# Performance work log

Hardware: AMD Instinct MI355X
Metric: run time of the kernel (lower is better)

## Reference

```python
import jax, jax.numpy as jnp
import numpy as np

NUM_HEADS = 8
AREA = 4
EPS = 1e-5  # torch BatchNorm2d default


def _conv1x1(x, w):
    # x: [B,C,H,W], w: [O,C] -> [B,O,H,W]
    return jnp.einsum('bchw,oc->bohw', x, w)


def _bn(y, g, b, m, v):
    # inference-mode BatchNorm2d, per-channel affine
    s = g / jnp.sqrt(v + EPS)
    return y * s[None, :, None, None] + (b - m * s)[None, :, None, None]


def setup_inputs() -> dict:
    key = jax.random.key(0)
    ks = jax.random.split(key, 16)
    B, C, H, W = 2, 256, 64, 64
    d = {}
    d['x'] = jax.random.normal(ks[0], (B, C, H, W), jnp.float32)
    # qk conv (dim -> 2*dim) + BN
    d['w_qk'] = jax.random.normal(ks[1], (2 * C, C), jnp.float32) * 0.06
    d['g_qk'] = jax.random.uniform(ks[2], (2 * C,), jnp.float32, 0.5, 1.5)
    d['b_qk'] = jax.random.normal(ks[3], (2 * C,), jnp.float32) * 0.1
    d['m_qk'] = jax.random.normal(ks[4], (2 * C,), jnp.float32) * 0.1
    d['v_qk'] = jax.random.uniform(ks[5], (2 * C,), jnp.float32, 0.5, 1.5)
    # v conv (dim -> dim) + BN
    d['w_v'] = jax.random.normal(ks[6], (C, C), jnp.float32) * 0.06
    d['g_v'] = jax.random.uniform(ks[7], (C,), jnp.float32, 0.5, 1.5)
    d['b_v'] = jax.random.normal(ks[8], (C,), jnp.float32) * 0.1
    d['m_v'] = jax.random.normal(ks[9], (C,), jnp.float32) * 0.1
    d['v_v'] = jax.random.uniform(ks[10], (C,), jnp.float32, 0.5, 1.5)
    # proj conv (dim -> dim) + BN
    d['w_p'] = jax.random.normal(ks[11], (C, C), jnp.float32) * 0.06
    d['g_p'] = jax.random.uniform(ks[12], (C,), jnp.float32, 0.5, 1.5)
    d['b_p'] = jax.random.normal(ks[13], (C,), jnp.float32) * 0.1
    d['m_p'] = jax.random.normal(ks[14], (C,), jnp.float32) * 0.1
    d['v_p'] = jax.random.uniform(ks[15], (C,), jnp.float32, 0.5, 1.5)
    return d


def reference(x, w_qk, g_qk, b_qk, m_qk, v_qk,
              w_v, g_v, b_v, m_v, v_v,
              w_p, g_p, b_p, m_p, v_p):
    B, C, H, W = x.shape
    N = H * W
    hd = C // NUM_HEADS

    qk = _bn(_conv1x1(x, w_qk), g_qk, b_qk, m_qk, v_qk)          # [B,2C,H,W]
    qk = qk.reshape(B, 2 * C, N).transpose(0, 2, 1)               # [B,N,2C]
    vv = _bn(_conv1x1(x, w_v), g_v, b_v, m_v, v_v)                # [B,C,H,W]
    vv = vv.reshape(B, C, N).transpose(0, 2, 1)                   # [B,N,C]

    Ba, Na = B * AREA, N // AREA
    qk = qk.reshape(Ba, Na, 2 * C)
    vv = vv.reshape(Ba, Na, C)
    q, k = qk[..., :C], qk[..., C:]

    # [Ba,Na,C] -> [Ba,heads,hd,Na] (matches torch transpose(1,2).view)
    q = q.reshape(Ba, Na, NUM_HEADS, hd).transpose(0, 2, 3, 1)
    k = k.reshape(Ba, Na, NUM_HEADS, hd).transpose(0, 2, 3, 1)
    v = vv.reshape(Ba, Na, NUM_HEADS, hd).transpose(0, 2, 3, 1)

    scale = hd ** -0.5
    attn = jnp.einsum('bhdi,bhdj->bhij', q, k) * scale            # [Ba,h,Na,Na]
    attn = jax.nn.softmax(attn, axis=-1)                          # max-sub exp/sum
    out = jnp.einsum('bhdj,bhij->bihd', v, attn)                  # [Ba,Na,h,hd]

    out = out.reshape(B, N, C).reshape(B, H, W, C).transpose(0, 3, 1, 2)
    return _bn(_conv1x1(out, w_p), g_p, b_p, m_p, v_p)            # [B,C,H,W]
```

## Files before the change

kernel.cpp:

```cpp
#include <hip/hip_runtime.h>
#include <hip/hip_bf16.h>
#include <math.h>

#define CCH   256
#define NPIX  4096
#define NHD   8
#define HD    32
#define NA    1024
#define BN_EPS 1e-5f
#define ATT_SCALE (0.17677669529663687f * 1.4426950408889634f)

typedef __attribute__((ext_vector_type(8))) short bf16x8;
typedef __attribute__((ext_vector_type(4))) short bf16x4;
typedef __attribute__((ext_vector_type(4))) float f32x4;

static __device__ inline short f2bf(float f) {
    union { float f; unsigned u; } v; v.f = f;
    unsigned r = (v.u + 0x7fff + ((v.u >> 16) & 1)) >> 16;
    return (short)r;
}

static __device__ inline unsigned int pk2bf(float a, float b) {
    __hip_bfloat162 h2 = __float22bfloat162_rn(make_float2(a, b));
    union { __hip_bfloat162 h; unsigned int u; } v; v.h = h2;
    return v.u;
}

__global__ __launch_bounds__(256)
void xt_kernel(const float* __restrict__ x, short* __restrict__ Xt) {
    __shared__ short tile[64][66];
    const int t  = threadIdx.x;
    const int n0 = blockIdx.x << 6;
    const int c0 = blockIdx.y << 6;
    const int b  = blockIdx.z;
    const float* xp = x + (((size_t)(b * CCH + c0)) << 12) + n0;
    #pragma unroll
    for (int j = 0; j < 16; ++j) {
        const int lin = (j << 8) + t;
        const int cl = lin >> 6, nl = lin & 63;
        tile[cl][nl] = f2bf(xp[((size_t)cl << 12) + nl]);
    }
    __syncthreads();
    short* xtp = Xt + ((((size_t)b << 12) + n0) << 8) + c0;
    #pragma unroll
    for (int j = 0; j < 16; ++j) {
        const int lin = (j << 8) + t;
        const int nl = lin >> 6, cl = lin & 63;
        xtp[((size_t)nl << 8) + cl] = tile[cl][nl];
    }
}

__global__ __launch_bounds__(256)
void wcast_kernel(const float* __restrict__ wqk, const float* __restrict__ wv,
                  const float* __restrict__ wp, short* __restrict__ Wb) {
    const int idx = (blockIdx.x * 256 + threadIdx.x) * 4;
    const float* src; int off;
    if (idx < 131072)      { src = wqk; off = idx; }
    else if (idx < 196608) { src = wv;  off = idx - 131072; }
    else                   { src = wp;  off = idx - 196608; }
    const float4 v = *(const float4*)(src + off);
    short4 o;
    o.x = f2bf(v.x); o.y = f2bf(v.y); o.z = f2bf(v.z); o.w = f2bf(v.w);
    *(short4*)(Wb + idx) = o;
}

__global__ __launch_bounds__(256)
void qk_gemm(const short* __restrict__ Xt, const short* __restrict__ Wb,
             const float* __restrict__ g_qk, const float* __restrict__ b_qk,
             const float* __restrict__ m_qk, const float* __restrict__ v_qk,
             short* __restrict__ Qb, short* __restrict__ Kb) {
    const int lane = threadIdx.x & 63;
    const int w    = threadIdx.x >> 6;
    const int c    = lane & 15;
    const int quad = lane >> 4;
    const int m0 = blockIdx.x * 64 + (w >> 1) * 32;
    const int n0 = blockIdx.y * 128 + (w & 1) * 64;

    const short* ap = Xt + ((size_t)(m0 + c) << 8) + (quad << 3);
    const short* bp = Wb + ((size_t)(n0 + c) << 8) + (quad << 3);

    f32x4 acc[2][4];
    #pragma unroll
    for (int f = 0; f < 2; ++f)
        #pragma unroll
        for (int g = 0; g < 4; ++g) acc[f][g] = (f32x4){0.f, 0.f, 0.f, 0.f};

    #pragma unroll
    for (int k = 0; k < 256; k += 32) {
        bf16x8 af[2], bg[4];
        #pragma unroll
        for (int f = 0; f < 2; ++f) af[f] = *(const bf16x8*)(ap + f * 4096 + k);
        #pragma unroll
        for (int g = 0; g < 4; ++g) bg[g] = *(const bf16x8*)(bp + g * 4096 + k);
        #pragma unroll
        for (int f = 0; f < 2; ++f)
            #pragma unroll
            for (int g = 0; g < 4; ++g)
                acc[f][g] = __builtin_amdgcn_mfma_f32_16x16x32_bf16(af[f], bg[g], acc[f][g], 0, 0, 0);
    }

    const bool isQ = (n0 < 256);
    short* dst = isQ ? Qb : Kb;
    const float fold = isQ ? ATT_SCALE : 1.0f;
    #pragma unroll
    for (int g = 0; g < 4; ++g) {
        const int o  = n0 + g * 16 + c;
        const int cd = o & 255;
        const int h  = cd >> 5;
        const int d  = cd & 31;
        float s    = g_qk[o] * rsqrtf(v_qk[o] + BN_EPS);
        float beta = (b_qk[o] - m_qk[o] * s) * fold;
        s *= fold;
        #pragma unroll
        for (int f = 0; f < 2; ++f) {
            #pragma unroll
            for (int r = 0; r < 4; ++r) {
                const int row  = m0 + f * 16 + (quad << 2) + r;
                const int pair = (row >> 10) * NHD + h;
                const int i    = row & 1023;
                dst[(((size_t)pair << 10) + i) * HD + d] = f2bf(acc[f][g][r] * s + beta);
            }
        }
    }
}

__global__ __launch_bounds__(256)
void v_gemm(const short* __restrict__ Wv, const short* __restrict__ Xt,
            const float* __restrict__ g_v, const float* __restrict__ b_v,
            const float* __restrict__ m_v, const float* __restrict__ v_v,
            short* __restrict__ Vb) {
    const int lane = threadIdx.x & 63;
    const int w    = threadIdx.x >> 6;
    const int c    = lane & 15;
    const int quad = lane >> 4;
    const int m0 = blockIdx.x * 64 + (w >> 1) * 32;
    const int n0 = blockIdx.y * 128 + (w & 1) * 64;

    const short* ap = Wv + ((size_t)(m0 + c) << 8) + (quad << 3);
    const short* bp = Xt + ((size_t)(n0 + c) << 8) + (quad << 3);

    f32x4 acc[2][4];
    #pragma unroll
    for (int f = 0; f < 2; ++f)
        #pragma unroll
        for (int g = 0; g < 4; ++g) acc[f][g] = (f32x4){0.f, 0.f, 0.f, 0.f};

    #pragma unroll
    for (int k = 0; k < 256; k += 32) {
        bf16x8 af[2], bg[4];
        #pragma unroll
        for (int f = 0; f < 2; ++f) af[f] = *(const bf16x8*)(ap + f * 4096 + k);
        #pragma unroll
        for (int g = 0; g < 4; ++g) bg[g] = *(const bf16x8*)(bp + g * 4096 + k);
        #pragma unroll
        for (int f = 0; f < 2; ++f)
            #pragma unroll
            for (int g = 0; g < 4; ++g)
                acc[f][g] = __builtin_amdgcn_mfma_f32_16x16x32_bf16(af[f], bg[g], acc[f][g], 0, 0, 0);
    }

    #pragma unroll
    for (int f = 0; f < 2; ++f) {
        #pragma unroll
        for (int r = 0; r < 4; ++r) {
            const int o = m0 + f * 16 + (quad << 2) + r;
            const float s    = g_v[o] * rsqrtf(v_v[o] + BN_EPS);
            const float beta = b_v[o] - m_v[o] * s;
            const int d = o & 31;
            const int hpair = o >> 5;
            #pragma unroll
            for (int g = 0; g < 4; ++g) {
                const int col  = n0 + g * 16 + c;
                const int pair = (col >> 10) * NHD + hpair;
                const int j    = col & 1023;
                Vb[((size_t)pair << 15) + (d << 10) + j] = f2bf(acc[f][g][r] * s + beta);
            }
        }
    }
}

__global__ __launch_bounds__(256, 4)
void attn_kernel(const short* __restrict__ Qb,
                 const short* __restrict__ Kb,
                 const short* __restrict__ Vb,
                 short* __restrict__ AOt) {
    const int tid  = threadIdx.x;
    const int wave = tid >> 6;
    const int lane = tid & 63;
    const int c    = lane & 15;
    const int quad = lane >> 4;
    const int pidx  = wave >> 1;
    const int jhalf = wave & 1;

    const int bx  = blockIdx.x;
    const int hi  = bx >> 3;
    const int p   = (bx & 7) + ((hi >> 4) << 3);
    const int blk = hi & 15;
    const int i0a = (blk << 6) + (pidx << 5);
    const int i0b = i0a + 16;
    const int ba  = p >> 3;
    const int h   = p & 7;

    __shared__ f32x4 mrgA[2][4][64];
    __shared__ float mrgL[2][2][64];

    const short* qbase = Qb + ((size_t)p << 15);
    const short* kbase = Kb + ((size_t)p << 15);
    const short* vbase = Vb + ((size_t)p << 15);

    bf16x8 qfa = *(const bf16x8*)(qbase + ((i0a + c) << 5) + (quad << 3));
    bf16x8 qfb = *(const bf16x8*)(qbase + ((i0b + c) << 5) + (quad << 3));

    const int perm = ((c >> 2) << 3) + (c & 3);
    const short* kp0 = kbase + (perm << 5) + (quad << 3);
    const short* kp1 = kp0 + 128;
    const short* vp0 = vbase + (c << 10) + (quad << 3);
    const short* vp1 = vbase + ((c + 16) << 10) + (quad << 3);

    f32x4 acc0a = {0.f,0.f,0.f,0.f}, acc1a = {0.f,0.f,0.f,0.f};
    f32x4 acc0b = {0.f,0.f,0.f,0.f}, acc1b = {0.f,0.f,0.f,0.f};
    float la = 0.f, lb = 0.f;
    const f32x4 zero = {0.f,0.f,0.f,0.f};

    const int jbeg = jhalf << 9;
    for (int jj = 0; jj < 512; jj += 32) {
        const int j0 = jbeg + jj;
        bf16x8 kf0 = *(const bf16x8*)(kp0 + (j0 << 5));
        bf16x8 kf1 = *(const bf16x8*)(kp1 + (j0 << 5));
        bf16x8 vf0 = *(const bf16x8*)(vp0 + j0);
        bf16x8 vf1 = *(const bf16x8*)(vp1 + j0);

        f32x4 s0a = __builtin_amdgcn_mfma_f32_16x16x32_bf16(kf0, qfa, zero, 0, 0, 0);
        f32x4 s1a = __builtin_amdgcn_mfma_f32_16x16x32_bf16(kf1, qfa, zero, 0, 0, 0);
        f32x4 s0b = __builtin_amdgcn_mfma_f32_16x16x32_bf16(kf0, qfb, zero, 0, 0, 0);
        f32x4 s1b = __builtin_amdgcn_mfma_f32_16x16x32_bf16(kf1, qfb, zero, 0, 0, 0);

        float p0a[4], p1a[4], p0b[4], p1b[4];
        #pragma unroll
        for (int r = 0; r < 4; ++r) {
            p0a[r] = __builtin_amdgcn_exp2f(s0a[r]);
            p1a[r] = __builtin_amdgcn_exp2f(s1a[r]);
            p0b[r] = __builtin_amdgcn_exp2f(s0b[r]);
            p1b[r] = __builtin_amdgcn_exp2f(s1b[r]);
        }
        la += (p0a[0]+p0a[1]) + (p0a[2]+p0a[3]) + (p1a[0]+p1a[1]) + (p1a[2]+p1a[3]);
        lb += (p0b[0]+p0b[1]) + (p0b[2]+p0b[3]) + (p1b[0]+p1b[1]) + (p1b[2]+p1b[3]);

        union { unsigned int u[4]; bf16x8 v; } pfa, pfb;
        pfa.u[0] = pk2bf(p0a[0], p0a[1]);
        pfa.u[1] = pk2bf(p0a[2], p0a[3]);
        pfa.u[2] = pk2bf(p1a[0], p1a[1]);
        pfa.u[3] = pk2bf(p1a[2], p1a[3]);
        pfb.u[0] = pk2bf(p0b[0], p0b[1]);
        pfb.u[1] = pk2bf(p0b[2], p0b[3]);
        pfb.u[2] = pk2bf(p1b[0], p1b[1]);
        pfb.u[3] = pk2bf(p1b[2], p1b[3]);

        acc0a = __builtin_amdgcn_mfma_f32_16x16x32_bf16(pfa.v, vf0, acc0a, 0, 0, 0);
        acc1a = __builtin_amdgcn_mfma_f32_16x16x32_bf16(pfa.v, vf1, acc1a, 0, 0, 0);
        acc0b = __builtin_amdgcn_mfma_f32_16x16x32_bf16(pfb.v, vf0, acc0b, 0, 0, 0);
        acc1b = __builtin_amdgcn_mfma_f32_16x16x32_bf16(pfb.v, vf1, acc1b, 0, 0, 0);
    }

    if (jhalf == 1) {
        mrgA[pidx][0][lane] = acc0a;
        mrgA[pidx][1][lane] = acc1a;
        mrgA[pidx][2][lane] = acc0b;
        mrgA[pidx][3][lane] = acc1b;
        mrgL[pidx][0][lane] = la;
        mrgL[pidx][1][lane] = lb;
    }
    __syncthreads();
    if (jhalf == 1) return;

    acc0a += mrgA[pidx][0][lane];
    acc1a += mrgA[pidx][1][lane];
    acc0b += mrgA[pidx][2][lane];
    acc1b += mrgA[pidx][3][lane];
    la += mrgL[pidx][0][lane];
    lb += mrgL[pidx][1][lane];

    la += __shfl_xor(la, 16); la += __shfl_xor(la, 32);
    lb += __shfl_xor(lb, 16); lb += __shfl_xor(lb, 32);

    #pragma unroll
    for (int r = 0; r < 4; ++r) {
        const int rr = (quad << 2) + r;
        const float rla = 1.f / __shfl(la, rr, 16);
        const float rlb = 1.f / __shfl(lb, rr, 16);
        const size_t basea = ((((size_t)ba << 10) + i0a + rr) << 8) + (h << 5);
        const size_t baseb = ((((size_t)ba << 10) + i0b + rr) << 8) + (h << 5);
        AOt[basea + c]      = f2bf(acc0a[r] * rla);
        AOt[basea + c + 16] = f2bf(acc1a[r] * rla);
        AOt[baseb + c]      = f2bf(acc0b[r] * rlb);
        AOt[baseb + c + 16] = f2bf(acc1b[r] * rlb);
    }
}

__global__ __launch_bounds__(256)
void pconv_gemm(const short* __restrict__ Wp, const short* __restrict__ AOt,
                const float* __restrict__ g_p, const float* __restrict__ b_p,
                const float* __restrict__ m_p, const float* __restrict__ v_p,
                float* __restrict__ out) {
    const int lane = threadIdx.x & 63;
    const int w    = threadIdx.x >> 6;
    const int c    = lane & 15;
    const int quad = lane >> 4;
    const int m0 = blockIdx.x * 64 + (w >> 1) * 32;
    const int n0 = blockIdx.y * 128 + (w & 1) * 64;

    const short* ap = Wp + ((size_t)(m0 + c) << 8) + (quad << 3);
    const short* bp = AOt + ((size_t)(n0 + c) << 8) + (quad << 3);

    f32x4 acc[2][4];
    #pragma unroll
    for (int f = 0; f < 2; ++f)
        #pragma unroll
        for (int g = 0; g < 4; ++g) acc[f][g] = (f32x4){0.f, 0.f, 0.f, 0.f};

    #pragma unroll
    for (int k = 0; k < 256; k += 32) {
        bf16x8 af[2], bg[4];
        #pragma unroll
        for (int f = 0; f < 2; ++f) af[f] = *(const bf16x8*)(ap + f * 4096 + k);
        #pragma unroll
        for (int g = 0; g < 4; ++g) bg[g] = *(const bf16x8*)(bp + g * 4096 + k);
        #pragma unroll
        for (int f = 0; f < 2; ++f)
            #pragma unroll
            for (int g = 0; g < 4; ++g)
                acc[f][g] = __builtin_amdgcn_mfma_f32_16x16x32_bf16(af[f], bg[g], acc[f][g], 0, 0, 0);
    }

    #pragma unroll
    for (int f = 0; f < 2; ++f) {
        #pragma unroll
        for (int r = 0; r < 4; ++r) {
            const int o = m0 + f * 16 + (quad << 2) + r;
            const float s    = g_p[o] * rsqrtf(v_p[o] + BN_EPS);
            const float beta = b_p[o] - m_p[o] * s;
            #pragma unroll
            for (int g = 0; g < 4; ++g) {
                const int col = n0 + g * 16 + c;
                const int b = col >> 12, n = col & 4095;
                out[((size_t)(b * CCH + o) << 12) + n] = acc[f][g][r] * s + beta;
            }
        }
    }
}

extern "C" void kernel_launch(void* const* d_in, const int* in_sizes, int n_in,
                              void* d_out, int out_size, void* d_ws, size_t ws_size,
                              hipStream_t stream) {
    const float* x    = (const float*)d_in[0];
    const float* w_qk = (const float*)d_in[1];
    const float* g_qk = (const float*)d_in[2];
    const float* b_qk = (const float*)d_in[3];
    const float* m_qk = (const float*)d_in[4];
    const float* v_qk = (const float*)d_in[5];
    const float* w_v  = (const float*)d_in[6];
    const float* g_v  = (const float*)d_in[7];
    const float* b_v  = (const float*)d_in[8];
    const float* m_v  = (const float*)d_in[9];
    const float* v_v  = (const float*)d_in[10];
    const float* w_p  = (const float*)d_in[11];
    const float* g_p  = (const float*)d_in[12];
    const float* b_p  = (const float*)d_in[13];
    const float* m_p  = (const float*)d_in[14];
    const float* v_p  = (const float*)d_in[15];

    short* Qb  = (short*)d_ws;
    short* Kb  = Qb + 2097152;
    short* Vb  = Kb + 2097152;
    short* Xt  = Vb + 2097152;
    short* Wb  = Xt + 2097152;
    short* AOt = Xt;

    dim3 gx(64, 4, 2);
    xt_kernel<<<gx, 256, 0, stream>>>(x, Xt);
    wcast_kernel<<<256, 256, 0, stream>>>(w_qk, w_v, w_p, Wb);

    dim3 gqk(128, 4);
    qk_gemm<<<gqk, 256, 0, stream>>>(Xt, Wb, g_qk, b_qk, m_qk, v_qk, Qb, Kb);
    dim3 gv(4, 64);
    v_gemm<<<gv, 256, 0, stream>>>(Wb + 512 * 256, Xt, g_v, b_v, m_v, v_v, Vb);

    attn_kernel<<<1024, 256, 0, stream>>>(Qb, Kb, Vb, AOt);

    dim3 gp(4, 64);
    pconv_gemm<<<gp, 256, 0, stream>>>(Wb + 768 * 256, AOt, g_p, b_p, m_p, v_p, (float*)d_out);
}
```

Measured before the change: 152.8 us.

## Split K across warps in the 1x1-conv GEMMs with shared-memory reduction

```diff
diff --git a/kernel.cpp b/kernel.cpp
--- a/kernel.cpp
+++ b/kernel.cpp
@@ -69,15 +69,20 @@
              const float* __restrict__ g_qk, const float* __restrict__ b_qk,
              const float* __restrict__ m_qk, const float* __restrict__ v_qk,
              short* __restrict__ Qb, short* __restrict__ Kb) {
-    const int lane = threadIdx.x & 63;
-    const int w    = threadIdx.x >> 6;
-    const int c    = lane & 15;
-    const int quad = lane >> 4;
-    const int m0 = blockIdx.x * 64 + (w >> 1) * 32;
-    const int n0 = blockIdx.y * 128 + (w & 1) * 64;
-
-    const short* ap = Xt + ((size_t)(m0 + c) << 8) + (quad << 3);
-    const short* bp = Wb + ((size_t)(n0 + c) << 8) + (quad << 3);
+    const int lane  = threadIdx.x & 63;
+    const int w     = threadIdx.x >> 6;
+    const int c     = lane & 15;
+    const int quad  = lane >> 4;
+    const int mpos  = w & 1;
+    const int khalf = w >> 1;
+    const int m0 = blockIdx.x * 64 + mpos * 32;
+    const int n0 = blockIdx.y * 64;
+    const int kb = khalf << 7;
+
+    __shared__ f32x4 mrg[2][8][64];
+
+    const short* ap = Xt + ((size_t)(m0 + c) << 8) + (quad << 3) + kb;
+    const short* bp = Wb + ((size_t)(n0 + c) << 8) + (quad << 3) + kb;
 
     f32x4 acc[2][4];
     #pragma unroll
@@ -86,7 +91,7 @@
         for (int g = 0; g < 4; ++g) acc[f][g] = (f32x4){0.f, 0.f, 0.f, 0.f};
 
     #pragma unroll
-    for (int k = 0; k < 256; k += 32) {
+    for (int k = 0; k < 128; k += 32) {
         bf16x8 af[2], bg[4];
         #pragma unroll
         for (int f = 0; f < 2; ++f) af[f] = *(const bf16x8*)(ap + f * 4096 + k);
@@ -98,6 +103,19 @@
             for (int g = 0; g < 4; ++g)
                 acc[f][g] = __builtin_amdgcn_mfma_f32_16x16x32_bf16(af[f], bg[g], acc[f][g], 0, 0, 0);
     }
+
+    if (khalf == 1) {
+        #pragma unroll
+        for (int f = 0; f < 2; ++f)
+            #pragma unroll
+            for (int g = 0; g < 4; ++g) mrg[mpos][f * 4 + g][lane] = acc[f][g];
+    }
+    __syncthreads();
+    if (khalf == 1) return;
+    #pragma unroll
+    for (int f = 0; f < 2; ++f)
+        #pragma unroll
+        for (int g = 0; g < 4; ++g) acc[f][g] += mrg[mpos][f * 4 + g][lane];
 
     const bool isQ = (n0 < 256);
     short* dst = isQ ? Qb : Kb;
@@ -133,11 +151,14 @@
     const int w    = threadIdx.x >> 6;
     const int c    = lane & 15;
     const int quad = lane >> 4;
-    const int m0 = blockIdx.x * 64 + (w >> 1) * 32;
-    const int n0 = blockIdx.y * 128 + (w & 1) * 64;
-
-    const short* ap = Wv + ((size_t)(m0 + c) << 8) + (quad << 3);
-    const short* bp = Xt + ((size_t)(n0 + c) << 8) + (quad << 3);
+    const int m0 = blockIdx.x * 32;
+    const int n0 = blockIdx.y * 64;
+    const int kb = w << 6;
+
+    __shared__ f32x4 mrg[3][8][64];
+
+    const short* ap = Wv + ((size_t)(m0 + c) << 8) + (quad << 3) + kb;
+    const short* bp = Xt + ((size_t)(n0 + c) << 8) + (quad << 3) + kb;
 
     f32x4 acc[2][4];
     #pragma unroll
@@ -146,7 +167,7 @@
         for (int g = 0; g < 4; ++g) acc[f][g] = (f32x4){0.f, 0.f, 0.f, 0.f};
 
     #pragma unroll
-    for (int k = 0; k < 256; k += 32) {
+    for (int k = 0; k < 64; k += 32) {
         bf16x8 af[2], bg[4];
         #pragma unroll
         for (int f = 0; f < 2; ++f) af[f] = *(const bf16x8*)(ap + f * 4096 + k);
@@ -158,6 +179,21 @@
             for (int g = 0; g < 4; ++g)
                 acc[f][g] = __builtin_amdgcn_mfma_f32_16x16x32_bf16(af[f], bg[g], acc[f][g], 0, 0, 0);
     }
+
+    if (w > 0) {
+        #pragma unroll
+        for (int f = 0; f < 2; ++f)
+            #pragma unroll
+            for (int g = 0; g < 4; ++g) mrg[w - 1][f * 4 + g][lane] = acc[f][g];
+    }
+    __syncthreads();
+    if (w > 0) return;
+    #pragma unroll
+    for (int q = 0; q < 3; ++q)
+        #pragma unroll
+        for (int f = 0; f < 2; ++f)
+            #pragma unroll
+            for (int g = 0; g < 4; ++g) acc[f][g] += mrg[q][f * 4 + g][lane];
 
     #pragma unroll
     for (int f = 0; f < 2; ++f) {
@@ -306,11 +342,14 @@
     const int w    = threadIdx.x >> 6;
     const int c    = lane & 15;
     const int quad = lane >> 4;
-    const int m0 = blockIdx.x * 64 + (w >> 1) * 32;
-    const int n0 = blockIdx.y * 128 + (w & 1) * 64;
-
-    const short* ap = Wp + ((size_t)(m0 + c) << 8) + (quad << 3);
-    const short* bp = AOt + ((size_t)(n0 + c) << 8) + (quad << 3);
+    const int m0 = blockIdx.x * 32;
+    const int n0 = blockIdx.y * 64;
+    const int kb = w << 6;
+
+    __shared__ f32x4 mrg[3][8][64];
+
+    const short* ap = Wp + ((size_t)(m0 + c) << 8) + (quad << 3) + kb;
+    const short* bp = AOt + ((size_t)(n0 + c) << 8) + (quad << 3) + kb;
 
     f32x4 acc[2][4];
     #pragma unroll
@@ -319,7 +358,7 @@
         for (int g = 0; g < 4; ++g) acc[f][g] = (f32x4){0.f, 0.f, 0.f, 0.f};
 
     #pragma unroll
-    for (int k = 0; k < 256; k += 32) {
+    for (int k = 0; k < 64; k += 32) {
         bf16x8 af[2], bg[4];
         #pragma unroll
         for (int f = 0; f < 2; ++f) af[f] = *(const bf16x8*)(ap + f * 4096 + k);
@@ -331,6 +370,21 @@
             for (int g = 0; g < 4; ++g)
                 acc[f][g] = __builtin_amdgcn_mfma_f32_16x16x32_bf16(af[f], bg[g], acc[f][g], 0, 0, 0);
     }
+
+    if (w > 0) {
+        #pragma unroll
+        for (int f = 0; f < 2; ++f)
+            #pragma unroll
+            for (int g = 0; g < 4; ++g) mrg[w - 1][f * 4 + g][lane] = acc[f][g];
+    }
+    __syncthreads();
+    if (w > 0) return;
+    #pragma unroll
+    for (int q = 0; q < 3; ++q)
+        #pragma unroll
+        for (int f = 0; f < 2; ++f)
+            #pragma unroll
+            for (int g = 0; g < 4; ++g) acc[f][g] += mrg[q][f * 4 + g][lane];
 
     #pragma unroll
     for (int f = 0; f < 2; ++f) {
@@ -380,13 +434,13 @@
     xt_kernel<<<gx, 256, 0, stream>>>(x, Xt);
     wcast_kernel<<<256, 256, 0, stream>>>(w_qk, w_v, w_p, Wb);
 
-    dim3 gqk(128, 4);
+    dim3 gqk(128, 8);
     qk_gemm<<<gqk, 256, 0, stream>>>(Xt, Wb, g_qk, b_qk, m_qk, v_qk, Qb, Kb);
-    dim3 gv(4, 64);
+    dim3 gv(8, 128);
     v_gemm<<<gv, 256, 0, stream>>>(Wb + 512 * 256, Xt, g_v, b_v, m_v, v_v, Vb);
 
     attn_kernel<<<1024, 256, 0, stream>>>(Qb, Kb, Vb, AOt);
 
-    dim3 gp(4, 64);
+    dim3 gp(8, 128);
     pconv_gemm<<<gp, 256, 0, stream>>>(Wb + 768 * 256, AOt, g_p, b_p, m_p, v_p, (float*)d_out);
 }
```

Measured after the change: 155.1 us. About the same (+1.5%).
